# Optimization experiments

Hardware: AMD Instinct MI355X
Metric: run time of the kernel (lower is better)

The kernel has to match this reference:

```python
import jax, jax.numpy as jnp
import numpy as np

N_HEADS = 16
D_K = 64
MAX_LEN = 5000


def setup_inputs() -> dict:
    key = jax.random.key(0)
    ks = jax.random.split(key, 6)
    B, L, D = 4, 1024, 1024
    s = 1.0 / np.sqrt(D).astype(np.float32)
    return {
        "x": jax.random.normal(ks[0], (B, L, D), jnp.float32),
        "W_q": jax.random.normal(ks[1], (D, D), jnp.float32) * s,
        "b_q": jnp.zeros((D,), jnp.float32),
        "W_k": jax.random.normal(ks[2], (D, D), jnp.float32) * s,
        "b_k": jnp.zeros((D,), jnp.float32),
        "W_v": jax.random.normal(ks[3], (D, D), jnp.float32) * s,
        "b_v": jnp.zeros((D,), jnp.float32),
        "W_o": jax.random.normal(ks[4], (D, D), jnp.float32) * s,
        "b_o": jnp.zeros((D,), jnp.float32),
        "Er": jax.random.normal(ks[5], (MAX_LEN, D_K), jnp.float32) * 0.02,
    }


def reference(x, W_q, b_q, W_k, b_k, W_v, b_v, W_o, b_o, Er):
    B, L, D = x.shape
    H = N_HEADS
    dk = D // H
    # torch nn.Linear: y = x @ W.T + b
    Q = (x @ W_q.T + b_q).reshape(B, L, H, dk).transpose(0, 2, 1, 3)  # (B,H,L,dk)
    K = (x @ W_k.T + b_k).reshape(B, L, H, dk).transpose(0, 2, 1, 3)
    V = (x @ W_v.T + b_v).reshape(B, L, H, dk).transpose(0, 2, 1, 3)
    AC = jnp.einsum('bhid,bhjd->bhij', Q, K)  # (B,H,L,L)
    rel_pos = jnp.arange(L - 1, -L, -1) + (MAX_LEN - 1)  # (2L-1,)
    # mode='clip' matches intended math: clamped rows fall in the part that
    # the relative shift slices away.
    Er_embed = jnp.take(Er, rel_pos, axis=0, mode='clip')  # (2L-1, dk)
    BD = jnp.einsum('bhid,rd->bhir', Q, Er_embed)  # (B,H,L,2L-1)
    # _relative_shift: view is a no-op (shape already (B,H,L,2L-1)), then slice
    BD = BD[..., L - 1:]  # (B,H,L,L)
    scores = (AC + BD) / np.sqrt(dk).astype(np.float32)
    attn = jax.nn.softmax(scores, axis=-1)
    out = jnp.einsum('bhij,bhjd->bhid', attn, V)
    out = out.transpose(0, 2, 1, 3).reshape(B, L, D)
    return out @ W_o.T + b_o
```

## Files before the change

kernel.cpp:

```cpp
#include <hip/hip_runtime.h>
#include <cstdint>
#include <cstddef>


typedef __attribute__((ext_vector_type(8))) short short8;
typedef __attribute__((ext_vector_type(4))) float f32x4;

#define MFMA_BF16(a, b, c) __builtin_amdgcn_mfma_f32_16x16x32_bf16((a), (b), (c), 0, 0, 0)

constexpr int kB = 4, kL = 1024, kD = 1024, kH = 16;
constexpr int kBL = kB * kL;
constexpr float kScale = 0.125f * 1.44269504088896340736f;

static __device__ __forceinline__ unsigned short f32_to_bf16(float f) {
  union { float f; uint32_t u; } c; c.f = f;
  uint32_t u = c.u + 0x7fffu + ((c.u >> 16) & 1u);
  return (unsigned short)(u >> 16);
}

static __device__ __forceinline__ void gload_lds16(const void* g, void* l) {
  __builtin_amdgcn_global_load_lds(
      (const __attribute__((address_space(1))) void*)g,
      (__attribute__((address_space(3))) void*)l, 16, 0, 0);
}

__global__ __launch_bounds__(256)
void cast_all(const float* __restrict__ x,  const float* __restrict__ Wq,
              const float* __restrict__ Wk, const float* __restrict__ Wv,
              const float* __restrict__ Wo,
              unsigned short* __restrict__ xb, unsigned short* __restrict__ Wcat,
              unsigned short* __restrict__ Wob) {
  int i = blockIdx.x * blockDim.x + threadIdx.x;
  const float* src;
  ushort4* dst;
  int off;
  if (i < 1048576) {
    src = x; dst = reinterpret_cast<ushort4*>(xb); off = i;
  } else {
    int j = i - 1048576;
    int seg = j >> 18;
    off = j & 262143;
    if (seg == 0)      { src = Wq; dst = reinterpret_cast<ushort4*>(Wcat); }
    else if (seg == 1) { src = Wk; dst = reinterpret_cast<ushort4*>(Wcat) + 262144; }
    else if (seg == 2) { src = Wv; dst = reinterpret_cast<ushort4*>(Wcat) + 524288; }
    else               { src = Wo; dst = reinterpret_cast<ushort4*>(Wob); }
  }
  float4 v = reinterpret_cast<const float4*>(src)[off];
  ushort4 o;
  o.x = f32_to_bf16(v.x); o.y = f32_to_bf16(v.y);
  o.z = f32_to_bf16(v.z); o.w = f32_to_bf16(v.w);
  dst[off] = o;
}

__global__ __launch_bounds__(512, 2)
void gemm_qkv(const unsigned short* __restrict__ A,
              const unsigned short* __restrict__ Bm,
              const float* __restrict__ bq, const float* __restrict__ bk,
              const float* __restrict__ bv,
              const float* __restrict__ Er,
              unsigned short* __restrict__ Qh, unsigned short* __restrict__ Kh,
              unsigned short* __restrict__ Vth) {
  __shared__ __align__(16) char smem[114688];
  const int tid  = threadIdx.x;
  const int lane = tid & 63, wave = tid >> 6;
  const int quad = lane >> 4, l15 = lane & 15;
  const int wr = wave >> 2, wc = wave & 3;

  const int bid = blockIdx.x;
  const int xcd = bid & 7, idx = bid >> 3;
  const int m0 = ((xcd >> 1) * 4 + (idx >> 3)) * 256;
  const int n0 = ((xcd & 1) * 8 + (idx & 7)) * 192;

  const int aoff = (l15 >> 1) * 128 + (l15 & 1) * 64 +
                   ((quad * 16) ^ (((l15 >> 1) & 3) << 4)) + wr * 8192;
  const int b_lane = (quad * 16) ^ ((l15 & 7) << 4);
  const int boff = (wc * 48 + l15) * 128 + b_lane;

  int srowA[2], scolA[2];
#pragma unroll
  for (int j = 0; j < 2; ++j) {
    int poff = (j * 512 + tid) * 16;
    int L = poff ^ (((poff >> 7) & 3) << 4);
    srowA[j] = ((L >> 7) << 1) | ((L >> 6) & 1);
    scolA[j] = (L & 63) >> 1;
  }
  int srowB[3], scolB[3];
#pragma unroll
  for (int j = 0; j < 3; ++j) {
    int poff = (j * 512 + tid) * 16;
    int L = poff ^ (((poff >> 7) & 7) << 4);
    srowB[j] = L >> 7;
    scolB[j] = (L & 127) >> 1;
  }

  auto stageA = [&](int kh, int tt) {
    char* dst = smem + (tt & 1) * 32768 + kh * 16384 + tid * 16;
    const int kc = tt * 64 + kh * 32;
#pragma unroll
    for (int j = 0; j < 2; ++j)
      gload_lds16(A + (size_t)(m0 + srowA[j]) * 1024 + kc + scolA[j],
                  dst + j * 8192);
  };
  auto stageB = [&](int tt) {
    char* dst = smem + 65536 + (tt & 1) * 24576 + tid * 16;
    const int kc = tt * 64;
#pragma unroll
    for (int j = 0; j < 3; ++j)
      gload_lds16(Bm + (size_t)(n0 + srowB[j]) * 1024 + kc + scolB[j],
                  dst + j * 8192);
  };

  const f32x4 vzero = {0.f, 0.f, 0.f, 0.f};
  f32x4 acc[8][3];
#pragma unroll
  for (int i = 0; i < 8; ++i)
#pragma unroll
    for (int j = 0; j < 3; ++j) acc[i][j] = vzero;

  stageA(0, 0); stageB(0); stageA(1, 0); stageA(0, 1);
  asm volatile("s_waitcnt vmcnt(4)" ::: "memory");
  __builtin_amdgcn_s_barrier();

#define LDA(KH, MB) do {                                                      \
    _Pragma("unroll")                                                         \
    for (int f_ = 0; f_ < 4; ++f_)                                            \
      af[f_] = *(const short8*)(RA + (KH) * 16384 + aoff + ((MB) + f_) * 1024); \
  } while (0)
#define LDB(KH) do {                                                          \
    _Pragma("unroll")                                                         \
    for (int n_ = 0; n_ < 3; ++n_)                                            \
      bf[n_] = *(const short8*)(RB + ((boff + n_ * 2048) ^ ((KH) * 64)));     \
  } while (0)
#define BARA() do {                                                           \
    __builtin_amdgcn_s_barrier();                                             \
    asm volatile("s_waitcnt lgkmcnt(0)" ::: "memory");                        \
    __builtin_amdgcn_sched_barrier(0);                                        \
  } while (0)
#define MFMA_12(MB) do {                                                      \
    __builtin_amdgcn_s_setprio(1);                                            \
    _Pragma("unroll")                                                         \
    for (int mq_ = 0; mq_ < 4; ++mq_) {                                       \
      _Pragma("unroll")                                                       \
      for (int nq_ = 0; nq_ < 3; ++nq_)                                       \
        acc[(MB) + mq_][nq_] =                                                \
            MFMA_BF16(af[mq_], bf[nq_], acc[(MB) + mq_][nq_]);                \
    }                                                                         \
    __builtin_amdgcn_s_setprio(0);                                            \
  } while (0)

  for (int t = 0; t < 16; ++t) {
    const char* RA = smem + (t & 1) * 32768;
    const char* RB = smem + 65536 + (t & 1) * 24576;
    short8 af[4], bf[3];
    LDA(0, 0); LDB(0);
    if (t + 1 < 16) stageB(t + 1);
    BARA(); MFMA_12(0);
    __builtin_amdgcn_s_barrier();
    LDA(0, 4);
    if (t + 1 < 16) stageA(1, t + 1);
    BARA(); MFMA_12(4);
    if (t < 15) asm volatile("s_waitcnt vmcnt(7)" ::: "memory");
    else        asm volatile("s_waitcnt vmcnt(0)" ::: "memory");
    __builtin_amdgcn_s_barrier();
    LDA(1, 0); LDB(1);
    if (t + 2 < 16) stageA(0, t + 2);
    BARA(); MFMA_12(0);
    __builtin_amdgcn_s_barrier();
    LDA(1, 4);
    BARA(); MFMA_12(4);
    if (t < 14)       asm volatile("s_waitcnt vmcnt(4)" ::: "memory");
    else if (t == 14) asm volatile("s_waitcnt vmcnt(2)" ::: "memory");
    else              asm volatile("s_waitcnt vmcnt(0)" ::: "memory");
    __builtin_amdgcn_s_barrier();
  }

#undef LDA
#undef LDB
#undef BARA
#undef MFMA_12

  __syncthreads();
  const int gmb = m0 + wr * 128;
  const int bb  = gmb >> 10, i0l = gmb & 1023;
  unsigned short* Wv = (unsigned short*)smem + (size_t)wave * 6144;

#pragma unroll
  for (int nf = 0; nf < 3; ++nf) {
    const int n    = n0 + wc * 48 + nf * 16;
    const int wsel = n >> 10;
    const int nin  = n & 1023;
    const int hh   = nin >> 6, d0 = nin & 63;
    const size_t bh = (size_t)(bb * 16 + hh);

    if (wsel == 0) {
#pragma unroll
      for (int mf = 0; mf < 8; ++mf)
#pragma unroll
        for (int r = 0; r < 4; ++r) {
          const int i = i0l + mf * 16 + quad * 4 + r;
          float v = (acc[mf][nf][r] + bq[nin + l15]) * kScale;
          Qh[(bh * 1024 + i) * 64 + d0 + l15] = f32_to_bf16(v);
        }
    } else if (wsel == 1) {
#pragma unroll
      for (int mf = 0; mf < 8; ++mf)
#pragma unroll
        for (int r = 0; r < 4; ++r) {
          const int i = i0l + mf * 16 + quad * 4 + r;
          float v = acc[mf][nf][r] + bk[nin + l15] +
                    Er[(size_t)(4999 - i) * 64 + d0 + l15];
          Kh[(bh * 1024 + i) * 64 + d0 + l15] = f32_to_bf16(v);
        }
    } else {
      unsigned short* Wn = Wv + nf * 2048;
#pragma unroll
      for (int mf = 0; mf < 8; ++mf) {
        ushort4 pk;
        pk.x = f32_to_bf16(acc[mf][nf][0] + bv[nin + l15]);
        pk.y = f32_to_bf16(acc[mf][nf][1] + bv[nin + l15]);
        pk.z = f32_to_bf16(acc[mf][nf][2] + bv[nin + l15]);
        pk.w = f32_to_bf16(acc[mf][nf][3] + bv[nin + l15]);
        *(ushort4*)&Wn[(size_t)l15 * 128 + mf * 16 + quad * 4] = pk;
      }
#pragma unroll
      for (int p = 0; p < 4; ++p) {
        const int u = p * 64 + lane;
        const int dl = u >> 4, ch = (u & 15) * 8;
        short8 vv = *(const short8*)&Wn[(size_t)dl * 128 + ch];
        *(short8*)&Vth[(bh * 64 + d0 + dl) * 1024 + i0l + ch] = vv;
      }
    }
  }
}

__global__ __launch_bounds__(256)
void gemm_out(const unsigned short* __restrict__ A,
              const unsigned short* __restrict__ Bm,
              const float* __restrict__ bias,
              float* __restrict__ outf) {
  __shared__ unsigned short As[2][128 * 32];
  __shared__ unsigned short Bs[2][64 * 32];
  const int tid  = threadIdx.x;
  const int lane = tid & 63, wave = tid >> 6;
  const int quad = lane >> 4, l15 = lane & 15;
  const int m0 = blockIdx.y * 128, n0 = blockIdx.x * 64;
  const int K = 1024;

  const f32x4 vzero = {0.f, 0.f, 0.f, 0.f};
  f32x4 acc[2][4];
#pragma unroll
  for (int i = 0; i < 2; ++i)
#pragma unroll
    for (int j = 0; j < 4; ++j) acc[i][j] = vzero;

  for (int k0 = 0; k0 < K; k0 += 64) {
    __syncthreads();
#pragma unroll
    for (int j = 0; j < 4; ++j) {
      int u = j * 256 + tid;
      int half = u >> 9, row = (u >> 2) & 127, c = (u & 3) * 8 + half * 32;
      gload_lds16(A + (size_t)(m0 + row) * K + k0 + c, (char*)&As[0][0] + (size_t)u * 16);
    }
#pragma unroll
    for (int j = 0; j < 2; ++j) {
      int u = j * 256 + tid;
      int half = u >> 8, row = (u >> 2) & 63, c = (u & 3) * 8 + half * 32;
      gload_lds16(Bm + (size_t)(n0 + row) * K + k0 + c, (char*)&Bs[0][0] + (size_t)u * 16);
    }
    __syncthreads();

#pragma unroll
    for (int ks = 0; ks < 2; ++ks) {
      short8 af[2], bfv[4];
#pragma unroll
      for (int mt = 0; mt < 2; ++mt)
        af[mt] = *(const short8*)&As[ks][(wave * 32 + mt * 16 + l15) * 32 + quad * 8];
#pragma unroll
      for (int nt = 0; nt < 4; ++nt)
        bfv[nt] = *(const short8*)&Bs[ks][(nt * 16 + l15) * 32 + quad * 8];
#pragma unroll
      for (int mt = 0; mt < 2; ++mt)
#pragma unroll
        for (int nt = 0; nt < 4; ++nt)
          acc[mt][nt] = MFMA_BF16(af[mt], bfv[nt], acc[mt][nt]);
    }
  }

#pragma unroll
  for (int mt = 0; mt < 2; ++mt)
#pragma unroll
    for (int nt = 0; nt < 4; ++nt)
#pragma unroll
      for (int r = 0; r < 4; ++r) {
        const int gm = m0 + wave * 32 + mt * 16 + quad * 4 + r;
        const int gn = n0 + nt * 16 + l15;
        outf[(size_t)gm * 1024 + gn] = acc[mt][nt][r] + bias[gn];
      }
}

__global__ __launch_bounds__(256)
void attn_kernel(const unsigned short* __restrict__ Q,
                 const unsigned short* __restrict__ Kp,
                 const unsigned short* __restrict__ Vt,
                 unsigned short* __restrict__ Ao) {
  __shared__ unsigned short Ks[2][2][64 * 32];
  __shared__ unsigned short Vs[2][2][64 * 32];
  __shared__ unsigned short Plds[4][32 * 72];
  const int tid  = threadIdx.x;
  const int lane = tid & 63, wave = tid >> 6;
  const int quad = lane >> 4, l15 = lane & 15;
  const int bh = blockIdx.x;
  const int qb = blockIdx.y;
  const size_t base  = (size_t)bh * (kL * 64);
  const size_t vbase = (size_t)bh * (64 * kL);
  const int i0 = qb * 128 + wave * 32;

  short8 qf[2][2];
#pragma unroll
  for (int mt = 0; mt < 2; ++mt)
#pragma unroll
    for (int ks = 0; ks < 2; ++ks)
      qf[mt][ks] = *(const short8*)
          &Q[base + (size_t)(i0 + mt * 16 + l15) * 64 + ks * 32 + quad * 8];

  auto stage = [&](int buf, int kb) {
#pragma unroll
    for (int j = 0; j < 2; ++j) {
      int u = j * 256 + tid;
      int half = u >> 8, row = (u >> 2) & 63, c = (u & 3) * 8;
      gload_lds16(Kp + base + (size_t)(kb * 64 + row) * 64 + half * 32 + c,
                  (char*)&Ks[buf][0][0] + (size_t)u * 16);
      gload_lds16(Vt + vbase + (size_t)row * kL + kb * 64 + half * 32 + c,
                  (char*)&Vs[buf][0][0] + (size_t)u * 16);
    }
  };

  const f32x4 vzero = {0.f, 0.f, 0.f, 0.f};
  f32x4 of[2][4];
#pragma unroll
  for (int mt = 0; mt < 2; ++mt)
#pragma unroll
    for (int dt = 0; dt < 4; ++dt) of[mt][dt] = vzero;
  float lsum[2][4] = {{0.f, 0.f, 0.f, 0.f}, {0.f, 0.f, 0.f, 0.f}};

  unsigned short* Pw = Plds[wave];

  stage(0, 0);
  __syncthreads();

  for (int kb = 0; kb < 16; ++kb) {
    const int cur = kb & 1, nxt = cur ^ 1;
    if (kb < 15) stage(nxt, kb + 1);

    short8 kf[4][2];
#pragma unroll
    for (int nt = 0; nt < 4; ++nt)
#pragma unroll
      for (int ks = 0; ks < 2; ++ks)
        kf[nt][ks] = *(const short8*)&Ks[cur][ks][(nt * 16 + l15) * 32 + quad * 8];
    f32x4 sf[2][4];
#pragma unroll
    for (int mt = 0; mt < 2; ++mt)
#pragma unroll
      for (int nt = 0; nt < 4; ++nt) {
        sf[mt][nt] = MFMA_BF16(qf[mt][0], kf[nt][0], vzero);
        sf[mt][nt] = MFMA_BF16(qf[mt][1], kf[nt][1], sf[mt][nt]);
      }

#pragma unroll
    for (int mt = 0; mt < 2; ++mt)
#pragma unroll
      for (int nt = 0; nt < 4; ++nt)
#pragma unroll
        for (int r = 0; r < 4; ++r) {
          float p = __builtin_amdgcn_exp2f(sf[mt][nt][r]);
          lsum[mt][r] += p;
          union { float f; uint32_t u; } c; c.f = p;
          Pw[(mt * 16 + quad * 4 + r) * 72 + nt * 16 + l15] =
              (unsigned short)((c.u + 0x8000u) >> 16);
        }
    short8 pf[2][2];
#pragma unroll
    for (int mt = 0; mt < 2; ++mt)
#pragma unroll
      for (int ks = 0; ks < 2; ++ks)
        pf[mt][ks] = *(const short8*)&Pw[(mt * 16 + l15) * 72 + ks * 32 + quad * 8];

    short8 vf[4][2];
#pragma unroll
    for (int dt = 0; dt < 4; ++dt)
#pragma unroll
      for (int ks = 0; ks < 2; ++ks)
        vf[dt][ks] = *(const short8*)&Vs[cur][ks][(dt * 16 + l15) * 32 + quad * 8];
#pragma unroll
    for (int mt = 0; mt < 2; ++mt)
#pragma unroll
      for (int dt = 0; dt < 4; ++dt) {
        of[mt][dt] = MFMA_BF16(pf[mt][0], vf[dt][0], of[mt][dt]);
        of[mt][dt] = MFMA_BF16(pf[mt][1], vf[dt][1], of[mt][dt]);
      }

    __syncthreads();
  }

#pragma unroll
  for (int mask = 1; mask < 16; mask <<= 1)
#pragma unroll
    for (int mt = 0; mt < 2; ++mt)
#pragma unroll
      for (int r = 0; r < 4; ++r)
        lsum[mt][r] += __shfl_xor(lsum[mt][r], mask);
  float rl[2][4];
#pragma unroll
  for (int mt = 0; mt < 2; ++mt)
#pragma unroll
    for (int r = 0; r < 4; ++r) rl[mt][r] = __builtin_amdgcn_rcpf(lsum[mt][r]);

  const int b = bh >> 4, h = bh & 15;
#pragma unroll
  for (int mt = 0; mt < 2; ++mt)
#pragma unroll
    for (int dt = 0; dt < 4; ++dt)
#pragma unroll
      for (int r = 0; r < 4; ++r) {
        const int ig = i0 + mt * 16 + quad * 4 + r;
        float v = of[mt][dt][r] * rl[mt][r];
        Ao[((size_t)(b * 1024 + ig)) * 1024 + h * 64 + dt * 16 + l15] = f32_to_bf16(v);
      }
}

extern "C" void kernel_launch(void* const* d_in, const int* in_sizes, int n_in,
                              void* d_out, int out_size, void* d_ws, size_t ws_size,
                              hipStream_t stream) {
  const float* x   = (const float*)d_in[0];
  const float* W_q = (const float*)d_in[1];
  const float* b_q = (const float*)d_in[2];
  const float* W_k = (const float*)d_in[3];
  const float* b_k = (const float*)d_in[4];
  const float* W_v = (const float*)d_in[5];
  const float* b_v = (const float*)d_in[6];
  const float* W_o = (const float*)d_in[7];
  const float* b_o = (const float*)d_in[8];
  const float* Er  = (const float*)d_in[9];
  float* out = (float*)d_out;

  char* ws = (char*)d_ws;
  unsigned short* xb   = (unsigned short*)(ws + (size_t)0);
  unsigned short* Wcat = (unsigned short*)(ws + ((size_t)8  << 20));
  unsigned short* Wob  = (unsigned short*)(ws + ((size_t)14 << 20));
  unsigned short* Qh   = (unsigned short*)(ws + ((size_t)16 << 20));
  unsigned short* Kh   = (unsigned short*)(ws + ((size_t)24 << 20));
  unsigned short* Vth  = (unsigned short*)(ws + ((size_t)32 << 20));
  unsigned short* Aoh  = (unsigned short*)(ws + ((size_t)40 << 20));

  cast_all<<<8192, 256, 0, stream>>>(x, W_q, W_k, W_v, W_o, xb, Wcat, Wob);

  gemm_qkv<<<256, 512, 0, stream>>>(
      xb, Wcat, b_q, b_k, b_v, Er, Qh, Kh, Vth);

  attn_kernel<<<dim3(kB * kH, kL / 128), 256, 0, stream>>>(Qh, Kh, Vth, Aoh);

  gemm_out<<<dim3(16, 32), 256, 0, stream>>>(Aoh, Wob, b_o, out);
}
```

Measured before the change: 173.4 us.

## Double-buffer and swizzle output GEMM LDS; transpose score MFMA for packed P stores

The output-projection GEMM now uses a double-buffered, XOR-swizzled LDS layout. The next tile's loads are issued before computing the current one, with explicit vmcnt waits and raw barriers, so global loads overlap MFMA work and LDS bank conflicts drop. In attention, the score MFMA operands are swapped so each lane holds four consecutive keys of one query row. This lets the probabilities be packed into 64-bit bf16 stores and replaces the 16-lane shuffle row-sum reduction with a two-step one plus a broadcast. The risks are correctness of the hand-written swizzle and waitcnt logic, and the extra LDS footprint.

```diff
diff --git a/kernel.cpp b/kernel.cpp
--- a/kernel.cpp
+++ b/kernel.cpp
@@ -16,6 +16,11 @@
   union { float f; uint32_t u; } c; c.f = f;
   uint32_t u = c.u + 0x7fffu + ((c.u >> 16) & 1u);
   return (unsigned short)(u >> 16);
+}
+
+static __device__ __forceinline__ uint32_t pack_bf16x2(float a, float b) {
+  union { float f; uint32_t u; } ca, cb; ca.f = a; cb.f = b;
+  return ((ca.u + 0x8000u) >> 16) | ((cb.u + 0x8000u) & 0xffff0000u);
 }
 
 static __device__ __forceinline__ void gload_lds16(const void* g, void* l) {
@@ -238,13 +243,52 @@
               const unsigned short* __restrict__ Bm,
               const float* __restrict__ bias,
               float* __restrict__ outf) {
-  __shared__ unsigned short As[2][128 * 32];
-  __shared__ unsigned short Bs[2][64 * 32];
+  __shared__ __align__(16) char smem[49152];
   const int tid  = threadIdx.x;
   const int lane = tid & 63, wave = tid >> 6;
   const int quad = lane >> 4, l15 = lane & 15;
   const int m0 = blockIdx.y * 128, n0 = blockIdx.x * 64;
-  const int K = 1024;
+
+  const int afo = (l15 >> 1) * 128 + (l15 & 1) * 64 +
+                  ((quad * 16) ^ (((l15 >> 1) & 3) << 4));
+
+  int arow[4], acol[4], akh[4];
+#pragma unroll
+  for (int j = 0; j < 4; ++j) {
+    int u = j * 256 + tid;
+    akh[j] = u >> 9;
+    int poff = (u & 511) * 16;
+    int L = poff ^ (((poff >> 7) & 3) << 4);
+    arow[j] = ((L >> 7) << 1) | ((L >> 6) & 1);
+    acol[j] = (L & 63) >> 1;
+  }
+  int brow[2], bcol[2], bkh[2];
+#pragma unroll
+  for (int j = 0; j < 2; ++j) {
+    int u = j * 256 + tid;
+    bkh[j] = u >> 8;
+    int poff = (u & 255) * 16;
+    int L = poff ^ (((poff >> 7) & 3) << 4);
+    brow[j] = ((L >> 7) << 1) | ((L >> 6) & 1);
+    bcol[j] = (L & 63) >> 1;
+  }
+
+  auto stageG = [&](int buf, int t) {
+    char* base = smem + buf * 24576;
+    const int kc = t * 64;
+#pragma unroll
+    for (int j = 0; j < 4; ++j) {
+      int u = j * 256 + tid;
+      gload_lds16(A + (size_t)(m0 + arow[j]) * 1024 + kc + akh[j] * 32 + acol[j],
+                  base + u * 16);
+    }
+#pragma unroll
+    for (int j = 0; j < 2; ++j) {
+      int u = j * 256 + tid;
+      gload_lds16(Bm + (size_t)(n0 + brow[j]) * 1024 + kc + bkh[j] * 32 + bcol[j],
+                  base + 16384 + u * 16);
+    }
+  };
 
   const f32x4 vzero = {0.f, 0.f, 0.f, 0.f};
   f32x4 acc[2][4];
@@ -253,37 +297,33 @@
 #pragma unroll
     for (int j = 0; j < 4; ++j) acc[i][j] = vzero;
 
-  for (int k0 = 0; k0 < K; k0 += 64) {
-    __syncthreads();
-#pragma unroll
-    for (int j = 0; j < 4; ++j) {
-      int u = j * 256 + tid;
-      int half = u >> 9, row = (u >> 2) & 127, c = (u & 3) * 8 + half * 32;
-      gload_lds16(A + (size_t)(m0 + row) * K + k0 + c, (char*)&As[0][0] + (size_t)u * 16);
-    }
-#pragma unroll
-    for (int j = 0; j < 2; ++j) {
-      int u = j * 256 + tid;
-      int half = u >> 8, row = (u >> 2) & 63, c = (u & 3) * 8 + half * 32;
-      gload_lds16(Bm + (size_t)(n0 + row) * K + k0 + c, (char*)&Bs[0][0] + (size_t)u * 16);
-    }
-    __syncthreads();
-
+  stageG(0, 0);
+  for (int t = 0; t < 16; ++t) {
+    const int cur = t & 1;
+    if (t < 15) stageG(cur ^ 1, t + 1);
+    if (t < 15) asm volatile("s_waitcnt vmcnt(6)" ::: "memory");
+    else        asm volatile("s_waitcnt vmcnt(0)" ::: "memory");
+    __builtin_amdgcn_s_barrier();
+    __builtin_amdgcn_sched_barrier(0);
+    const char* Ab = smem + cur * 24576;
+    const char* Bb = Ab + 16384;
 #pragma unroll
     for (int ks = 0; ks < 2; ++ks) {
       short8 af[2], bfv[4];
 #pragma unroll
       for (int mt = 0; mt < 2; ++mt)
-        af[mt] = *(const short8*)&As[ks][(wave * 32 + mt * 16 + l15) * 32 + quad * 8];
+        af[mt] = *(const short8*)(Ab + ks * 8192 + wave * 2048 + mt * 1024 + afo);
 #pragma unroll
       for (int nt = 0; nt < 4; ++nt)
-        bfv[nt] = *(const short8*)&Bs[ks][(nt * 16 + l15) * 32 + quad * 8];
+        bfv[nt] = *(const short8*)(Bb + ks * 4096 + nt * 1024 + afo);
 #pragma unroll
       for (int mt = 0; mt < 2; ++mt)
 #pragma unroll
         for (int nt = 0; nt < 4; ++nt)
           acc[mt][nt] = MFMA_BF16(af[mt], bfv[nt], acc[mt][nt]);
     }
+    __builtin_amdgcn_s_barrier();
+    __builtin_amdgcn_sched_barrier(0);
   }
 
 #pragma unroll
@@ -341,7 +381,7 @@
   for (int mt = 0; mt < 2; ++mt)
 #pragma unroll
     for (int dt = 0; dt < 4; ++dt) of[mt][dt] = vzero;
-  float lsum[2][4] = {{0.f, 0.f, 0.f, 0.f}, {0.f, 0.f, 0.f, 0.f}};
+  float lsum[2] = {0.f, 0.f};
 
   unsigned short* Pw = Plds[wave];
 
@@ -363,22 +403,24 @@
     for (int mt = 0; mt < 2; ++mt)
 #pragma unroll
       for (int nt = 0; nt < 4; ++nt) {
-        sf[mt][nt] = MFMA_BF16(qf[mt][0], kf[nt][0], vzero);
-        sf[mt][nt] = MFMA_BF16(qf[mt][1], kf[nt][1], sf[mt][nt]);
+        sf[mt][nt] = MFMA_BF16(kf[nt][0], qf[mt][0], vzero);
+        sf[mt][nt] = MFMA_BF16(kf[nt][1], qf[mt][1], sf[mt][nt]);
       }
 
 #pragma unroll
     for (int mt = 0; mt < 2; ++mt)
 #pragma unroll
-      for (int nt = 0; nt < 4; ++nt)
-#pragma unroll
-        for (int r = 0; r < 4; ++r) {
-          float p = __builtin_amdgcn_exp2f(sf[mt][nt][r]);
-          lsum[mt][r] += p;
-          union { float f; uint32_t u; } c; c.f = p;
-          Pw[(mt * 16 + quad * 4 + r) * 72 + nt * 16 + l15] =
-              (unsigned short)((c.u + 0x8000u) >> 16);
-        }
+      for (int nt = 0; nt < 4; ++nt) {
+        float p0 = __builtin_amdgcn_exp2f(sf[mt][nt][0]);
+        float p1 = __builtin_amdgcn_exp2f(sf[mt][nt][1]);
+        float p2 = __builtin_amdgcn_exp2f(sf[mt][nt][2]);
+        float p3 = __builtin_amdgcn_exp2f(sf[mt][nt][3]);
+        lsum[mt] += (p0 + p1) + (p2 + p3);
+        uint2 w;
+        w.x = pack_bf16x2(p0, p1);
+        w.y = pack_bf16x2(p2, p3);
+        *(uint2*)&Pw[(mt * 16 + l15) * 72 + nt * 16 + quad * 4] = w;
+      }
     short8 pf[2][2];
 #pragma unroll
     for (int mt = 0; mt < 2; ++mt)
@@ -403,18 +445,16 @@
     __syncthreads();
   }
 
-#pragma unroll
-  for (int mask = 1; mask < 16; mask <<= 1)
-#pragma unroll
-    for (int mt = 0; mt < 2; ++mt)
-#pragma unroll
-      for (int r = 0; r < 4; ++r)
-        lsum[mt][r] += __shfl_xor(lsum[mt][r], mask);
   float rl[2][4];
 #pragma unroll
-  for (int mt = 0; mt < 2; ++mt)
-#pragma unroll
-    for (int r = 0; r < 4; ++r) rl[mt][r] = __builtin_amdgcn_rcpf(lsum[mt][r]);
+  for (int mt = 0; mt < 2; ++mt) {
+    float s = lsum[mt];
+    s += __shfl_xor(s, 16);
+    s += __shfl_xor(s, 32);
+#pragma unroll
+    for (int r = 0; r < 4; ++r)
+      rl[mt][r] = __builtin_amdgcn_rcpf(__shfl(s, quad * 4 + r));
+  }
 
   const int b = bh >> 4, h = bh & 15;
 #pragma unroll
```

Result: no change. 172.1 us (-0.7%).
